# Kernel optimization log

Hardware: AMD Instinct MI355X
Metric: run time of the kernel (lower is better)

Reference implementation:

```python
import jax, jax.numpy as jnp
import numpy as np

B, T, DIN, D = 8, 2048, 512, 1024
LN_EPS = 1e-5


def setup_inputs() -> dict:
    key = jax.random.key(0)
    k0, k1, k2, k3 = jax.random.split(key, 4)
    x = jax.random.normal(k0, (B, T, DIN), jnp.float32)
    # Linear params (torch layout: W [out, in]); delta_proj bias is zero-init per module
    Wd = jax.random.normal(k1, (D, DIN), jnp.float32) / np.sqrt(DIN)
    bd = jnp.zeros((D,), jnp.float32)
    Wb = jax.random.normal(k2, (D, DIN), jnp.float32) / np.sqrt(DIN)
    bb = jax.random.normal(k3, (D,), jnp.float32) * 0.01
    A_log = jnp.log(jnp.linspace(1.0, 16.0, D, dtype=jnp.float32))
    threshold = jnp.ones((D,), jnp.float32)
    gamma = jnp.ones((D,), jnp.float32)
    beta = jnp.zeros((D,), jnp.float32)
    h0 = jnp.zeros((B, D), jnp.float32)
    return {"x": x, "Wd": Wd, "bd": bd, "Wb": Wb, "bb": bb,
            "A_log": A_log, "threshold": threshold,
            "gamma": gamma, "beta": beta, "h0": h0}


def reference(x, Wd, bd, Wb, bb, A_log, threshold, gamma, beta, h0):
    # Input-dependent step parameters (computed once, outside the scan)
    delta = jax.nn.softplus(jnp.einsum('btc,dc->btd', x, Wd) + bd)   # [B,T,D]
    b_step = delta * (jnp.einsum('btc,dc->btd', x, Wb) + bb)          # [B,T,D]
    A_step = jnp.exp(-delta * jnp.exp(A_log))                         # [B,T,D]

    def step(h, ab):
        a, b = ab                      # each [B,D]
        h = a * h + b
        s = (h - threshold > 0).astype(x.dtype)   # spike (non-differentiable)
        h = h * (1.0 - s)                          # hard reset
        return h, (h, s)

    # scan over time: move T to the leading axis
    _, (h_post, spikes) = jax.lax.scan(
        step, h0, (A_step.transpose(1, 0, 2), b_step.transpose(1, 0, 2)))
    h_post = h_post.transpose(1, 0, 2)   # [B,T,D]
    spikes = spikes.transpose(1, 0, 2)   # [B,T,D]

    # LayerNorm over last dim
    mu = jnp.mean(h_post, axis=-1, keepdims=True)
    var = jnp.mean(jnp.square(h_post - mu), axis=-1, keepdims=True)
    out = (h_post - mu) * jax.lax.rsqrt(var + LN_EPS) * gamma + beta
    return (out, spikes)
```

## Files before the change

### kernel.cpp

```cpp
#include <hip/hip_runtime.h>
#include <cmath>

constexpr int Bb  = 8;
constexpr int Tt  = 2048;
constexpr int DIN = 512;
constexpr int Dd  = 1024;
constexpr long long BT  = (long long)Bb * Tt;
constexpr long long BTD = BT * Dd;

__device__ __forceinline__ float np_expf(float x) {
  const float LOG2E = 1.4426950408889634074f;
  const float MAGIC = 12582912.0f;
  const float C1 = -6.93145752e-1f;
  const float C2 = -1.42860677e-6f;
  const float P0 = 9.999999999980870924916e-01f;
  const float P1 = 7.257664613233124478488e-01f;
  const float P2 = 2.473615434895520810817e-01f;
  const float P3 = 5.114512081637298353406e-02f;
  const float P4 = 6.757896990527504603057e-03f;
  const float P5 = 5.082762527590693718096e-04f;
  const float Q0 = 1.0f;
  const float Q1 = -2.742335390411667452936e-01f;
  const float Q2 = 2.159509375685829852307e-02f;
  const float XMAX = 88.72283935546875f;
  const float XMIN = -87.3365478515625f;
  if (!(x == x)) return x;
  if (x > XMAX)  return __builtin_inff();
  if (x < XMIN)  return 0.0f;
  float q = __fsub_rn(fmaf(x, LOG2E, MAGIC), MAGIC);
  float r = fmaf(q, C1, x);
  r = fmaf(q, C2, r);
  float num = fmaf(r, P5, P4);
  num = fmaf(num, r, P3);
  num = fmaf(num, r, P2);
  num = fmaf(num, r, P1);
  num = fmaf(num, r, P0);
  float den = fmaf(r, Q2, Q1);
  den = fmaf(den, r, Q0);
  float p = __fdiv_rn(num, den);
  return ldexpf(p, (int)q);
}

__device__ __forceinline__ float expf_cr(float x) { return (float)exp((double)x); }

__device__ __forceinline__ float log1pf_fd(float x) {
  const float ln2_hi = __int_as_float(0x3f317180);
  const float ln2_lo = __int_as_float(0x3717f7d1);
  const float Lp1 = __int_as_float(0x3F2AAAAB), Lp2 = __int_as_float(0x3ECCCCCD),
              Lp3 = __int_as_float(0x3E924925), Lp4 = __int_as_float(0x3E638E29),
              Lp5 = __int_as_float(0x3E3A3325), Lp6 = __int_as_float(0x3E1CD04F),
              Lp7 = __int_as_float(0x3E178897);
  int hx = __float_as_int(x);
  int ax = hx & 0x7fffffff;
  int k = 1, hu = 0;
  float f = 0.f, c = 0.f, u;
  if (hx < 0x3ed413d7) {
    if (ax < 0x38000000) {
      if (ax < 0x33800000) return x;
      return __fsub_rn(x, __fmul_rn(__fmul_rn(x, x), 0.5f));
    }
    if (hx > 0 || hx <= (int)0xbe95f61f) { k = 0; f = x; hu = 1; }
  }
  if (k != 0) {
    if (hx < 0x4b800000) {
      u = __fadd_rn(1.0f, x);
      int hu0 = __float_as_int(u);
      k = (hu0 >> 23) - 127;
      c = (k > 0) ? __fsub_rn(1.0f, __fsub_rn(u, x))
                  : __fsub_rn(x, __fsub_rn(u, 1.0f));
      c = __fdiv_rn(c, u);
      hu = hu0;
    } else {
      u = x; hu = __float_as_int(u); k = (hu >> 23) - 127; c = 0.f;
    }
    hu &= 0x007fffff;
    if (hu < 0x3504f7) { u = __int_as_float(hu | 0x3f800000); }
    else { k += 1; u = __int_as_float(hu | 0x3f000000); hu = (0x00800000 - hu) >> 2; }
    f = __fsub_rn(u, 1.0f);
  }
  float hfsq = __fmul_rn(__fmul_rn(0.5f, f), f);
  if (hu == 0) {
    if (f == 0.0f) {
      if (k == 0) return 0.0f;
      c = __fadd_rn(c, __fmul_rn((float)k, ln2_lo));
      return __fadd_rn(__fmul_rn((float)k, ln2_hi), c);
    }
    float R = __fmul_rn(hfsq, __fsub_rn(1.0f, __fmul_rn(0.66666668653f, f)));
    if (k == 0) return __fsub_rn(f, R);
    return __fsub_rn(__fmul_rn((float)k, ln2_hi),
           __fsub_rn(__fsub_rn(R, __fadd_rn(__fmul_rn((float)k, ln2_lo), c)), f));
  }
  float s = __fdiv_rn(f, __fadd_rn(2.0f, f));
  float z = __fmul_rn(s, s);
  float pz = __fadd_rn(Lp6, __fmul_rn(z, Lp7));
  pz = __fadd_rn(Lp5, __fmul_rn(z, pz));
  pz = __fadd_rn(Lp4, __fmul_rn(z, pz));
  pz = __fadd_rn(Lp3, __fmul_rn(z, pz));
  pz = __fadd_rn(Lp2, __fmul_rn(z, pz));
  pz = __fadd_rn(Lp1, __fmul_rn(z, pz));
  float R = __fmul_rn(z, pz);
  if (k == 0)
    return __fsub_rn(f, __fsub_rn(hfsq, __fmul_rn(s, __fadd_rn(hfsq, R))));
  return __fsub_rn(__fmul_rn((float)k, ln2_hi),
         __fsub_rn(__fsub_rn(hfsq, __fadd_rn(__fmul_rn(s, __fadd_rn(hfsq, R)),
                   __fadd_rn(__fmul_rn((float)k, ln2_lo), c))), f));
}

__device__ __forceinline__ float np_softplus(float x) {
  if (x == 0.0f) return __int_as_float(0x3F317218);
  if (x > 0.0f)  return __fadd_rn(x, log1pf_fd(expf_cr(-x)));
  return log1pf_fd(expf_cr(x));
}

#define BM 128
#define BN 64
#define BK 32

__global__ __launch_bounds__(256) void gemm_np(
    const float* __restrict__ x,  const float* __restrict__ Wd,
    const float* __restrict__ bd, const float* __restrict__ Wb,
    const float* __restrict__ bb, const float* __restrict__ A_log,
    float* __restrict__ Aarr, float* __restrict__ Barr)
{
  __shared__ float xs[BM][BK];
  __shared__ float wds[BK][BN];
  __shared__ float wbs[BK][BN];

  const int tid = threadIdx.x;
  const int bn0 = blockIdx.x * BN;
  const int bm0 = blockIdx.y * BM;
  const int tx  = tid & 15;
  const int mg  = tid >> 4;
  const int swz = mg & 7;

  float accd[8][4], accb[8][4];
#pragma unroll
  for (int i = 0; i < 8; ++i)
#pragma unroll
    for (int j = 0; j < 4; ++j) { accd[i][j] = 0.f; accb[i][j] = 0.f; }

  for (int kt = 0; kt < DIN / BK; ++kt) {
    const int k0 = kt * BK;
    __syncthreads();
#pragma unroll
    for (int p = 0; p < 4; ++p) {
      int f   = p * 256 + tid;
      int row = f >> 3;
      int q   = f & 7;
      float4 v = *(const float4*)&x[(size_t)(bm0 + row) * DIN + k0 + q * 4];
      int qs = q ^ ((row >> 3) & 7);
      *(float4*)&xs[row][qs * 4] = v;
    }
#pragma unroll
    for (int p = 0; p < 2; ++p) {
      int f  = p * 256 + tid;
      int kq = f & 7;
      int n  = f >> 3;
      const size_t goff = (size_t)(bn0 + n) * DIN + k0 + kq * 4;
      float4 vd = *(const float4*)&Wd[goff];
      float4 vb = *(const float4*)&Wb[goff];
      wds[kq*4+0][n] = vd.x; wds[kq*4+1][n] = vd.y;
      wds[kq*4+2][n] = vd.z; wds[kq*4+3][n] = vd.w;
      wbs[kq*4+0][n] = vb.x; wbs[kq*4+1][n] = vb.y;
      wbs[kq*4+2][n] = vb.z; wbs[kq*4+3][n] = vb.w;
    }
    __syncthreads();

#pragma unroll
    for (int kq = 0; kq < BK / 4; ++kq) {
      float xk[8][4];
#pragma unroll
      for (int i = 0; i < 8; ++i) {
        float4 v = *(const float4*)&xs[mg * 8 + i][(kq ^ swz) * 4];
        xk[i][0] = v.x; xk[i][1] = v.y; xk[i][2] = v.z; xk[i][3] = v.w;
      }
#pragma unroll
      for (int t = 0; t < 4; ++t) {
        float4 wdv = *(const float4*)&wds[kq * 4 + t][tx * 4];
        float4 wbv = *(const float4*)&wbs[kq * 4 + t][tx * 4];
        float wd4[4] = {wdv.x, wdv.y, wdv.z, wdv.w};
        float wb4[4] = {wbv.x, wbv.y, wbv.z, wbv.w};
#pragma unroll
        for (int i = 0; i < 8; ++i) {
          const float xv = xk[i][t];
#pragma unroll
          for (int j = 0; j < 4; ++j) {
            accd[i][j] = __fadd_rn(accd[i][j], __fmul_rn(xv, wd4[j]));
            accb[i][j] = __fadd_rn(accb[i][j], __fmul_rn(xv, wb4[j]));
          }
        }
      }
    }
  }

  const int n0 = bn0 + tx * 4;
  float bd4[4], bb4[4], eA4[4];
#pragma unroll
  for (int j = 0; j < 4; ++j) {
    bd4[j] = bd[n0 + j];
    bb4[j] = bb[n0 + j];
    eA4[j] = np_expf(A_log[n0 + j]);
  }
#pragma unroll
  for (int i = 0; i < 8; ++i) {
    const int m = bm0 + mg * 8 + i;
    float av[4], bv[4];
#pragma unroll
    for (int j = 0; j < 4; ++j) {
      float z1b = __fadd_rn(accd[i][j], bd4[j]);
      float z2b = __fadd_rn(accb[i][j], bb4[j]);
      float delta = np_softplus(z1b);
      float w  = __fmul_rn(delta, eA4[j]);
      av[j] = np_expf(-w);
      bv[j] = __fmul_rn(delta, z2b);
    }
    *(float4*)&Aarr[(size_t)m * Dd + n0] = make_float4(av[0], av[1], av[2], av[3]);
    *(float4*)&Barr[(size_t)m * Dd + n0] = make_float4(bv[0], bv[1], bv[2], bv[3]);
  }
}

__global__ __launch_bounds__(64) void scan_np(
    const float* __restrict__ thr_arr, const float* __restrict__ h0,
    float* __restrict__ Aarr, float* __restrict__ Barr)
{
  const int bx = blockIdx.x;
  const int b  = bx >> 4;
  const int d  = ((bx & 15) << 6) + threadIdx.x;

  const float thr = thr_arr[d];
  float h = h0[(size_t)b * Dd + d];

  float* Ap = Aarr + (size_t)b * Tt * Dd + d;
  float* Bp = Barr + (size_t)b * Tt * Dd + d;

  constexpr int PF = 32;
  float pa[PF], pb[PF];
#pragma unroll
  for (int k = 0; k < PF; ++k) {
    pa[k] = Ap[(size_t)k * Dd];
    pb[k] = Bp[(size_t)k * Dd];
  }

  for (int t0 = 0; t0 < Tt; t0 += PF) {
    const int t1 = t0 + PF;
    float na[PF], nb[PF];
    if (t1 < Tt) {
#pragma unroll
      for (int k = 0; k < PF; ++k) {
        na[k] = Ap[(size_t)(t1 + k) * Dd];
        nb[k] = Bp[(size_t)(t1 + k) * Dd];
      }
    }
#pragma unroll
    for (int k = 0; k < PF; ++k) {
      h = __fadd_rn(__fmul_rn(pa[k], h), pb[k]);
      const bool spike = __fsub_rn(h, thr) > 0.0f;
      h = spike ? 0.0f : h;
      Ap[(size_t)(t0 + k) * Dd] = h;
      Bp[(size_t)(t0 + k) * Dd] = spike ? 1.0f : 0.0f;
    }
    if (t1 < Tt) {
#pragma unroll
      for (int k = 0; k < PF; ++k) { pa[k] = na[k]; pb[k] = nb[k]; }
    }
  }
}

__global__ __launch_bounds__(256) void ln_np(
    const float* __restrict__ gamma, const float* __restrict__ beta,
    float* __restrict__ H)
{
  const int row = blockIdx.x;
  const int tid = threadIdx.x;
  const size_t base = (size_t)row * Dd + (tid << 2);

  float4 v = *(const float4*)&H[base];

  __shared__ double red[4];
  __shared__ double red2[4];
  const int wave = tid >> 6, lane = tid & 63;

  double sum = (double)v.x + (double)v.y + (double)v.z + (double)v.w;
#pragma unroll
  for (int off = 32; off > 0; off >>= 1) sum += __shfl_down(sum, off);
  if (lane == 0) red[wave] = sum;
  __syncthreads();
  const float muf = (float)((red[0] + red[1] + red[2] + red[3]) * (1.0 / Dd));

  float dx0 = __fsub_rn(v.x, muf), dx1 = __fsub_rn(v.y, muf);
  float dx2 = __fsub_rn(v.z, muf), dx3 = __fsub_rn(v.w, muf);
  double sq = (double)dx0*dx0 + (double)dx1*dx1 + (double)dx2*dx2 + (double)dx3*dx3;
#pragma unroll
  for (int off = 32; off > 0; off >>= 1) sq += __shfl_down(sq, off);
  if (lane == 0) red2[wave] = sq;
  __syncthreads();
  const float varf = (float)((red2[0] + red2[1] + red2[2] + red2[3]) * (1.0 / Dd));
  const float invf = __fdiv_rn(1.0f, __fsqrt_rn(__fadd_rn(varf, 1e-5f)));

  const int n = tid << 2;
  float4 g  = *(const float4*)&gamma[n];
  float4 be = *(const float4*)&beta[n];
  float4 o;
  o.x = __fadd_rn(__fmul_rn(__fmul_rn(dx0, invf), g.x), be.x);
  o.y = __fadd_rn(__fmul_rn(__fmul_rn(dx1, invf), g.y), be.y);
  o.z = __fadd_rn(__fmul_rn(__fmul_rn(dx2, invf), g.z), be.z);
  o.w = __fadd_rn(__fmul_rn(__fmul_rn(dx3, invf), g.w), be.w);
  *(float4*)&H[base] = o;
}

extern "C" void kernel_launch(void* const* d_in, const int* in_sizes, int n_in,
                              void* d_out, int out_size, void* d_ws, size_t ws_size,
                              hipStream_t stream)
{
  const float* x     = (const float*)d_in[0];
  const float* Wd    = (const float*)d_in[1];
  const float* bd    = (const float*)d_in[2];
  const float* Wb    = (const float*)d_in[3];
  const float* bb    = (const float*)d_in[4];
  const float* A_log = (const float*)d_in[5];
  const float* thr   = (const float*)d_in[6];
  const float* gamma = (const float*)d_in[7];
  const float* beta  = (const float*)d_in[8];
  const float* h0    = (const float*)d_in[9];

  float* out  = (float*)d_out;
  float* Aarr = out;
  float* Barr = out + (size_t)BTD;

  dim3 g1(Dd / BN, (int)(BT / BM));
  gemm_np<<<g1, 256, 0, stream>>>(x, Wd, bd, Wb, bb, A_log, Aarr, Barr);
  scan_np<<<128, 64, 0, stream>>>(thr, h0, Aarr, Barr);
  ln_np<<<(int)BT, 256, 0, stream>>>(gamma, beta, Aarr);
}
```

Baseline: 675.2 us.

## Enlarge GEMM tile to 128x128 with 8x8 microtile and transposed swizzled LDS

Doubles the N tile of the fused projection GEMM and gives each thread an 8x8 output microtile, storing x transposed in shared memory with XOR swizzles so each k step needs only float4 loads. This raises arithmetic intensity per shared-memory load and halves the number of blocks that reload x. It doubles accumulator registers to 128 per thread, which may force spills or lower occupancy despite the launch-bounds hint. The grid launch must match the new BN.

```diff
diff --git a/kernel.cpp b/kernel.cpp
--- a/kernel.cpp
+++ b/kernel.cpp
@@ -113,16 +113,16 @@
 }
 
 #define BM 128
-#define BN 64
+#define BN 128
 #define BK 32
 
-__global__ __launch_bounds__(256) void gemm_np(
+__global__ __launch_bounds__(256, 2) void gemm_np(
     const float* __restrict__ x,  const float* __restrict__ Wd,
     const float* __restrict__ bd, const float* __restrict__ Wb,
     const float* __restrict__ bb, const float* __restrict__ A_log,
     float* __restrict__ Aarr, float* __restrict__ Barr)
 {
-  __shared__ float xs[BM][BK];
+  __shared__ float xsT[BK][BM];
   __shared__ float wds[BK][BN];
   __shared__ float wbs[BK][BN];
 
@@ -131,91 +131,103 @@
   const int bm0 = blockIdx.y * BM;
   const int tx  = tid & 15;
   const int mg  = tid >> 4;
-  const int swz = mg & 7;
-
-  float accd[8][4], accb[8][4];
+
+  const int wn    = tid & 127;
+  const int whalf = tid >> 7;
+
+  float accd[8][8], accb[8][8];
 #pragma unroll
   for (int i = 0; i < 8; ++i)
 #pragma unroll
-    for (int j = 0; j < 4; ++j) { accd[i][j] = 0.f; accb[i][j] = 0.f; }
+    for (int j = 0; j < 8; ++j) { accd[i][j] = 0.f; accb[i][j] = 0.f; }
 
   for (int kt = 0; kt < DIN / BK; ++kt) {
     const int k0 = kt * BK;
     __syncthreads();
 #pragma unroll
     for (int p = 0; p < 4; ++p) {
-      int f   = p * 256 + tid;
-      int row = f >> 3;
-      int q   = f & 7;
-      float4 v = *(const float4*)&x[(size_t)(bm0 + row) * DIN + k0 + q * 4];
-      int qs = q ^ ((row >> 3) & 7);
-      *(float4*)&xs[row][qs * 4] = v;
-    }
-#pragma unroll
-    for (int p = 0; p < 2; ++p) {
-      int f  = p * 256 + tid;
-      int kq = f & 7;
-      int n  = f >> 3;
-      const size_t goff = (size_t)(bn0 + n) * DIN + k0 + kq * 4;
-      float4 vd = *(const float4*)&Wd[goff];
-      float4 vb = *(const float4*)&Wb[goff];
-      wds[kq*4+0][n] = vd.x; wds[kq*4+1][n] = vd.y;
-      wds[kq*4+2][n] = vd.z; wds[kq*4+3][n] = vd.w;
-      wbs[kq*4+0][n] = vb.x; wbs[kq*4+1][n] = vb.y;
-      wbs[kq*4+2][n] = vb.z; wbs[kq*4+3][n] = vb.w;
+      int f = p * 256 + tid;
+      int m = f >> 3;
+      int q = f & 7;
+      float4 v = *(const float4*)&x[(size_t)(bm0 + m) * DIN + k0 + q * 4];
+      int col = m ^ (q << 3);
+      xsT[q*4+0][col] = v.x;
+      xsT[q*4+1][col] = v.y;
+      xsT[q*4+2][col] = v.z;
+      xsT[q*4+3][col] = v.w;
+    }
+#pragma unroll
+    for (int p = 0; p < 4; ++p) {
+      int kq = whalf * 4 + p;
+      const size_t g = (size_t)(bn0 + wn) * DIN + k0 + kq * 4;
+      float4 vd = *(const float4*)&Wd[g];
+      float4 vb = *(const float4*)&Wb[g];
+      int col = (((wn >> 2) ^ kq) << 2) | (wn & 3);
+      wds[kq*4+0][col] = vd.x; wds[kq*4+1][col] = vd.y;
+      wds[kq*4+2][col] = vd.z; wds[kq*4+3][col] = vd.w;
+      wbs[kq*4+0][col] = vb.x; wbs[kq*4+1][col] = vb.y;
+      wbs[kq*4+2][col] = vb.z; wbs[kq*4+3][col] = vb.w;
     }
     __syncthreads();
 
-#pragma unroll
+#pragma unroll 2
     for (int kq = 0; kq < BK / 4; ++kq) {
-      float xk[8][4];
-#pragma unroll
-      for (int i = 0; i < 8; ++i) {
-        float4 v = *(const float4*)&xs[mg * 8 + i][(kq ^ swz) * 4];
-        xk[i][0] = v.x; xk[i][1] = v.y; xk[i][2] = v.z; xk[i][3] = v.w;
-      }
+      const int xc0 = (mg * 8)     ^ (kq << 3);
+      const int xc1 = (mg * 8 + 4) ^ (kq << 3);
+      const int wc0 = ((tx * 2)     ^ kq) << 2;
+      const int wc1 = ((tx * 2 + 1) ^ kq) << 2;
 #pragma unroll
       for (int t = 0; t < 4; ++t) {
-        float4 wdv = *(const float4*)&wds[kq * 4 + t][tx * 4];
-        float4 wbv = *(const float4*)&wbs[kq * 4 + t][tx * 4];
-        float wd4[4] = {wdv.x, wdv.y, wdv.z, wdv.w};
-        float wb4[4] = {wbv.x, wbv.y, wbv.z, wbv.w};
+        const int k = kq * 4 + t;
+        float4 x0 = *(const float4*)&xsT[k][xc0];
+        float4 x1 = *(const float4*)&xsT[k][xc1];
+        float4 d0 = *(const float4*)&wds[k][wc0];
+        float4 d1 = *(const float4*)&wds[k][wc1];
+        float4 b0 = *(const float4*)&wbs[k][wc0];
+        float4 b1 = *(const float4*)&wbs[k][wc1];
+        float xa[8]  = {x0.x, x0.y, x0.z, x0.w, x1.x, x1.y, x1.z, x1.w};
+        float wd8[8] = {d0.x, d0.y, d0.z, d0.w, d1.x, d1.y, d1.z, d1.w};
+        float wb8[8] = {b0.x, b0.y, b0.z, b0.w, b1.x, b1.y, b1.z, b1.w};
 #pragma unroll
         for (int i = 0; i < 8; ++i) {
-          const float xv = xk[i][t];
-#pragma unroll
-          for (int j = 0; j < 4; ++j) {
-            accd[i][j] = __fadd_rn(accd[i][j], __fmul_rn(xv, wd4[j]));
-            accb[i][j] = __fadd_rn(accb[i][j], __fmul_rn(xv, wb4[j]));
+          const float xv = xa[i];
+#pragma unroll
+          for (int j = 0; j < 8; ++j) {
+            accd[i][j] = __fadd_rn(accd[i][j], __fmul_rn(xv, wd8[j]));
+            accb[i][j] = __fadd_rn(accb[i][j], __fmul_rn(xv, wb8[j]));
           }
         }
       }
     }
   }
 
-  const int n0 = bn0 + tx * 4;
-  float bd4[4], bb4[4], eA4[4];
-#pragma unroll
-  for (int j = 0; j < 4; ++j) {
-    bd4[j] = bd[n0 + j];
-    bb4[j] = bb[n0 + j];
-    eA4[j] = np_expf(A_log[n0 + j]);
+  const int n0 = bn0 + tx * 8;
+  float bd8[8], bb8[8], eA8[8];
+#pragma unroll
+  for (int j = 0; j < 8; ++j) {
+    bd8[j] = bd[n0 + j];
+    bb8[j] = bb[n0 + j];
+    eA8[j] = np_expf(A_log[n0 + j]);
   }
 #pragma unroll
   for (int i = 0; i < 8; ++i) {
     const int m = bm0 + mg * 8 + i;
-    float av[4], bv[4];
-#pragma unroll
-    for (int j = 0; j < 4; ++j) {
-      float z1b = __fadd_rn(accd[i][j], bd4[j]);
-      float z2b = __fadd_rn(accb[i][j], bb4[j]);
+    float av[8], bv[8];
+#pragma unroll
+    for (int j = 0; j < 8; ++j) {
+      float z1b = __fadd_rn(accd[i][j], bd8[j]);
+      float z2b = __fadd_rn(accb[i][j], bb8[j]);
       float delta = np_softplus(z1b);
-      float w  = __fmul_rn(delta, eA4[j]);
+      float w  = __fmul_rn(delta, eA8[j]);
       av[j] = np_expf(-w);
       bv[j] = __fmul_rn(delta, z2b);
     }
-    *(float4*)&Aarr[(size_t)m * Dd + n0] = make_float4(av[0], av[1], av[2], av[3]);
-    *(float4*)&Barr[(size_t)m * Dd + n0] = make_float4(bv[0], bv[1], bv[2], bv[3]);
+    float* Ap = &Aarr[(size_t)m * Dd + n0];
+    float* Bp = &Barr[(size_t)m * Dd + n0];
+    *(float4*)(Ap)     = make_float4(av[0], av[1], av[2], av[3]);
+    *(float4*)(Ap + 4) = make_float4(av[4], av[5], av[6], av[7]);
+    *(float4*)(Bp)     = make_float4(bv[0], bv[1], bv[2], bv[3]);
+    *(float4*)(Bp + 4) = make_float4(bv[4], bv[5], bv[6], bv[7]);
   }
 }
 
```

Result: slower. 696.9 us (+3.2%).

## Prefetch next GEMM tile into registers and swizzle weight shared-memory layout

Applied to the files above, without the earlier changes.

The fused projection GEMM now issues the global loads for the next K-tile into registers right after the shared-memory barrier. This lets them overlap the FMA loop on the current tile instead of stalling at the top of each iteration. The transposed weight tiles are stored with an XOR column swizzle, read back with the matching index, to reduce LDS bank conflicts on the scalar transpose stores. A launch-bounds occupancy hint of 4 blocks is added, which may push the compiler to limit registers while the prefetch buffers raise register pressure, risking spills.

```diff
diff --git a/kernel.cpp b/kernel.cpp
--- a/kernel.cpp
+++ b/kernel.cpp
@@ -116,7 +116,7 @@
 #define BN 64
 #define BK 32
 
-__global__ __launch_bounds__(256) void gemm_np(
+__global__ __launch_bounds__(256, 4) void gemm_np(
     const float* __restrict__ x,  const float* __restrict__ Wd,
     const float* __restrict__ bd, const float* __restrict__ Wb,
     const float* __restrict__ bb, const float* __restrict__ A_log,
@@ -133,38 +133,56 @@
   const int mg  = tid >> 4;
   const int swz = mg & 7;
 
+  const int sr8 = tid >> 3;
+  const int sq  = tid & 7;
+
   float accd[8][4], accb[8][4];
 #pragma unroll
   for (int i = 0; i < 8; ++i)
 #pragma unroll
     for (int j = 0; j < 4; ++j) { accd[i][j] = 0.f; accb[i][j] = 0.f; }
 
+  float4 px0, px1, px2, px3, pd0, pd1, pb0, pb1;
+#define ISSUE_LOADS(K0)                                                        \
+  {                                                                            \
+    const int k0_ = (K0);                                                      \
+    px0 = *(const float4*)&x[(size_t)(bm0 +  0 + sr8) * DIN + k0_ + sq * 4];   \
+    px1 = *(const float4*)&x[(size_t)(bm0 + 32 + sr8) * DIN + k0_ + sq * 4];   \
+    px2 = *(const float4*)&x[(size_t)(bm0 + 64 + sr8) * DIN + k0_ + sq * 4];   \
+    px3 = *(const float4*)&x[(size_t)(bm0 + 96 + sr8) * DIN + k0_ + sq * 4];   \
+    pd0 = *(const float4*)&Wd[(size_t)(bn0 +  0 + sr8) * DIN + k0_ + sq * 4];  \
+    pd1 = *(const float4*)&Wd[(size_t)(bn0 + 32 + sr8) * DIN + k0_ + sq * 4];  \
+    pb0 = *(const float4*)&Wb[(size_t)(bn0 +  0 + sr8) * DIN + k0_ + sq * 4];  \
+    pb1 = *(const float4*)&Wb[(size_t)(bn0 + 32 + sr8) * DIN + k0_ + sq * 4];  \
+  }
+
+  ISSUE_LOADS(0);
+
   for (int kt = 0; kt < DIN / BK; ++kt) {
-    const int k0 = kt * BK;
     __syncthreads();
-#pragma unroll
-    for (int p = 0; p < 4; ++p) {
-      int f   = p * 256 + tid;
-      int row = f >> 3;
-      int q   = f & 7;
-      float4 v = *(const float4*)&x[(size_t)(bm0 + row) * DIN + k0 + q * 4];
-      int qs = q ^ ((row >> 3) & 7);
-      *(float4*)&xs[row][qs * 4] = v;
-    }
-#pragma unroll
-    for (int p = 0; p < 2; ++p) {
-      int f  = p * 256 + tid;
-      int kq = f & 7;
-      int n  = f >> 3;
-      const size_t goff = (size_t)(bn0 + n) * DIN + k0 + kq * 4;
-      float4 vd = *(const float4*)&Wd[goff];
-      float4 vb = *(const float4*)&Wb[goff];
-      wds[kq*4+0][n] = vd.x; wds[kq*4+1][n] = vd.y;
-      wds[kq*4+2][n] = vd.z; wds[kq*4+3][n] = vd.w;
-      wbs[kq*4+0][n] = vb.x; wbs[kq*4+1][n] = vb.y;
-      wbs[kq*4+2][n] = vb.z; wbs[kq*4+3][n] = vb.w;
+    {
+      int r0 = sr8,      qs0 = sq ^ ((r0 >> 3) & 7);
+      int r1 = 32 + sr8, qs1 = sq ^ ((r1 >> 3) & 7);
+      int r2 = 64 + sr8, qs2 = sq ^ ((r2 >> 3) & 7);
+      int r3 = 96 + sr8, qs3 = sq ^ ((r3 >> 3) & 7);
+      *(float4*)&xs[r0][qs0 * 4] = px0;
+      *(float4*)&xs[r1][qs1 * 4] = px1;
+      *(float4*)&xs[r2][qs2 * 4] = px2;
+      *(float4*)&xs[r3][qs3 * 4] = px3;
+      int c0 = (sr8)      ^ (sq << 2);
+      int c1 = (32 + sr8) ^ (sq << 2);
+      wds[sq*4+0][c0] = pd0.x; wds[sq*4+1][c0] = pd0.y;
+      wds[sq*4+2][c0] = pd0.z; wds[sq*4+3][c0] = pd0.w;
+      wds[sq*4+0][c1] = pd1.x; wds[sq*4+1][c1] = pd1.y;
+      wds[sq*4+2][c1] = pd1.z; wds[sq*4+3][c1] = pd1.w;
+      wbs[sq*4+0][c0] = pb0.x; wbs[sq*4+1][c0] = pb0.y;
+      wbs[sq*4+2][c0] = pb0.z; wbs[sq*4+3][c0] = pb0.w;
+      wbs[sq*4+0][c1] = pb1.x; wbs[sq*4+1][c1] = pb1.y;
+      wbs[sq*4+2][c1] = pb1.z; wbs[sq*4+3][c1] = pb1.w;
     }
     __syncthreads();
+
+    if (kt + 1 < DIN / BK) ISSUE_LOADS((kt + 1) * BK);
 
 #pragma unroll
     for (int kq = 0; kq < BK / 4; ++kq) {
@@ -174,10 +192,11 @@
         float4 v = *(const float4*)&xs[mg * 8 + i][(kq ^ swz) * 4];
         xk[i][0] = v.x; xk[i][1] = v.y; xk[i][2] = v.z; xk[i][3] = v.w;
       }
+      const int wc = 4 * (tx ^ kq);
 #pragma unroll
       for (int t = 0; t < 4; ++t) {
-        float4 wdv = *(const float4*)&wds[kq * 4 + t][tx * 4];
-        float4 wbv = *(const float4*)&wbs[kq * 4 + t][tx * 4];
+        float4 wdv = *(const float4*)&wds[kq * 4 + t][wc];
+        float4 wbv = *(const float4*)&wbs[kq * 4 + t][wc];
         float wd4[4] = {wdv.x, wdv.y, wdv.z, wdv.w};
         float wb4[4] = {wbv.x, wbv.y, wbv.z, wbv.w};
 #pragma unroll
@@ -192,6 +211,7 @@
       }
     }
   }
+#undef ISSUE_LOADS
 
   const int n0 = bn0 + tx * 4;
   float bd4[4], bb4[4], eA4[4];
```

Result: slower. 1.360 ms (+101.5%).

## Double-buffer GEMM tiles with async global-to-LDS loads and XOR-swizzled weight layout

Applied to the files above, without the earlier changes.

Replaces the register-staged global-to-shared copies in the fused dual GEMM with __builtin_amdgcn_global_load_lds direct-to-LDS transfers into double-buffered shared tiles. The next K tile is prefetched while the current one is computed, hiding global load latency and removing the per-element transpose stores. Weight tiles get an XOR swizzle on the column index to avoid LDS bank conflicts. In exchange, LDS use doubles and the weights are fetched with 4-byte async loads, which may be inefficient.

```diff
diff --git a/kernel.cpp b/kernel.cpp
--- a/kernel.cpp
+++ b/kernel.cpp
@@ -116,15 +116,24 @@
 #define BN 64
 #define BK 32
 
+typedef const __attribute__((address_space(1))) void* gas1_t;
+typedef __attribute__((address_space(3))) void* las3_t;
+__device__ __forceinline__ void async16(const float* g, float* l) {
+  __builtin_amdgcn_global_load_lds((gas1_t)g, (las3_t)l, 16, 0, 0);
+}
+__device__ __forceinline__ void async4(const float* g, float* l) {
+  __builtin_amdgcn_global_load_lds((gas1_t)g, (las3_t)l, 4, 0, 0);
+}
+
 __global__ __launch_bounds__(256) void gemm_np(
     const float* __restrict__ x,  const float* __restrict__ Wd,
     const float* __restrict__ bd, const float* __restrict__ Wb,
     const float* __restrict__ bb, const float* __restrict__ A_log,
     float* __restrict__ Aarr, float* __restrict__ Barr)
 {
-  __shared__ float xs[BM][BK];
-  __shared__ float wds[BK][BN];
-  __shared__ float wbs[BK][BN];
+  __shared__ float xs[2][BM][BK];
+  __shared__ float wds[2][BK][BN];
+  __shared__ float wbs[2][BK][BN];
 
   const int tid = threadIdx.x;
   const int bn0 = blockIdx.x * BN;
@@ -132,6 +141,34 @@
   const int tx  = tid & 15;
   const int mg  = tid >> 4;
   const int swz = mg & 7;
+  const int w   = tid >> 6;
+  const int l   = tid & 63;
+
+  int xsrc[4];
+#pragma unroll
+  for (int i = 0; i < 4; ++i) {
+    int fidx = w * 256 + i * 64 + l;
+    int row  = fidx >> 3;
+    int q    = (fidx & 7) ^ ((row >> 3) & 7);
+    xsrc[i]  = (bm0 + row) * DIN + q * 4;
+  }
+  int wsrc[8];
+#pragma unroll
+  for (int j = 0; j < 8; ++j) {
+    int k   = w * 8 + j;
+    int n   = l ^ ((k >> 2) << 2);
+    wsrc[j] = (bn0 + n) * DIN + k;
+  }
+
+#define STAGE(b, K0)                                                         \
+  {                                                                          \
+    for (int i_ = 0; i_ < 4; ++i_)                                           \
+      async16(&x[xsrc[i_] + (K0)], &xs[b][0][0] + (w * 256 + i_ * 64) * 4);  \
+    for (int j_ = 0; j_ < 8; ++j_) {                                         \
+      async4(&Wd[wsrc[j_] + (K0)], &wds[b][0][0] + w * 512 + j_ * 64);       \
+      async4(&Wb[wsrc[j_] + (K0)], &wbs[b][0][0] + w * 512 + j_ * 64);       \
+    }                                                                        \
+  }
 
   float accd[8][4], accb[8][4];
 #pragma unroll
@@ -139,45 +176,27 @@
 #pragma unroll
     for (int j = 0; j < 4; ++j) { accd[i][j] = 0.f; accb[i][j] = 0.f; }
 
+  STAGE(0, 0);
+  asm volatile("s_waitcnt vmcnt(0)" ::: "memory");
+  __syncthreads();
+
   for (int kt = 0; kt < DIN / BK; ++kt) {
-    const int k0 = kt * BK;
-    __syncthreads();
-#pragma unroll
-    for (int p = 0; p < 4; ++p) {
-      int f   = p * 256 + tid;
-      int row = f >> 3;
-      int q   = f & 7;
-      float4 v = *(const float4*)&x[(size_t)(bm0 + row) * DIN + k0 + q * 4];
-      int qs = q ^ ((row >> 3) & 7);
-      *(float4*)&xs[row][qs * 4] = v;
-    }
-#pragma unroll
-    for (int p = 0; p < 2; ++p) {
-      int f  = p * 256 + tid;
-      int kq = f & 7;
-      int n  = f >> 3;
-      const size_t goff = (size_t)(bn0 + n) * DIN + k0 + kq * 4;
-      float4 vd = *(const float4*)&Wd[goff];
-      float4 vb = *(const float4*)&Wb[goff];
-      wds[kq*4+0][n] = vd.x; wds[kq*4+1][n] = vd.y;
-      wds[kq*4+2][n] = vd.z; wds[kq*4+3][n] = vd.w;
-      wbs[kq*4+0][n] = vb.x; wbs[kq*4+1][n] = vb.y;
-      wbs[kq*4+2][n] = vb.z; wbs[kq*4+3][n] = vb.w;
-    }
-    __syncthreads();
+    const int cb = kt & 1;
+    if (kt + 1 < DIN / BK) STAGE((kt + 1) & 1, (kt + 1) * BK);
 
 #pragma unroll
     for (int kq = 0; kq < BK / 4; ++kq) {
       float xk[8][4];
 #pragma unroll
       for (int i = 0; i < 8; ++i) {
-        float4 v = *(const float4*)&xs[mg * 8 + i][(kq ^ swz) * 4];
+        float4 v = *(const float4*)&xs[cb][mg * 8 + i][(kq ^ swz) * 4];
         xk[i][0] = v.x; xk[i][1] = v.y; xk[i][2] = v.z; xk[i][3] = v.w;
       }
+      const int wc = 4 * (tx ^ kq);
 #pragma unroll
       for (int t = 0; t < 4; ++t) {
-        float4 wdv = *(const float4*)&wds[kq * 4 + t][tx * 4];
-        float4 wbv = *(const float4*)&wbs[kq * 4 + t][tx * 4];
+        float4 wdv = *(const float4*)&wds[cb][kq * 4 + t][wc];
+        float4 wbv = *(const float4*)&wbs[cb][kq * 4 + t][wc];
         float wd4[4] = {wdv.x, wdv.y, wdv.z, wdv.w};
         float wb4[4] = {wbv.x, wbv.y, wbv.z, wbv.w};
 #pragma unroll
@@ -191,7 +210,13 @@
         }
       }
     }
-  }
+
+    if (kt + 1 < DIN / BK) {
+      asm volatile("s_waitcnt vmcnt(0)" ::: "memory");
+      __syncthreads();
+    }
+  }
+#undef STAGE
 
   const int n0 = bn0 + tx * 4;
   float bd4[4], bb4[4], eA4[4];
@@ -210,8 +235,8 @@
       float z1b = __fadd_rn(accd[i][j], bd4[j]);
       float z2b = __fadd_rn(accb[i][j], bb4[j]);
       float delta = np_softplus(z1b);
-      float w  = __fmul_rn(delta, eA4[j]);
-      av[j] = np_expf(-w);
+      float w2 = __fmul_rn(delta, eA4[j]);
+      av[j] = np_expf(-w2);
       bv[j] = __fmul_rn(delta, z2b);
     }
     *(float4*)&Aarr[(size_t)m * Dd + n0] = make_float4(av[0], av[1], av[2], av[3]);
```

After: 2.580 ms. 3.82x slower.
